# Performance work log

Hardware: AMD Instinct MI355X
Metric: run time of the kernel (lower is better)

The kernel has to match this reference:

```python
import jax, jax.numpy as jnp
import numpy as np

D_MODEL = 1024
NUM_HEADS = 16
HEAD_DIM = D_MODEL // NUM_HEADS
B, L = 2, 2048


def apply_rope(x, pos_emb):
    # x: [B,H,L,Dh], pos_emb: [1,1,L,Dh]
    x_even = x[..., ::2]
    x_odd = x[..., 1::2]
    cos = pos_emb[..., ::2]
    sin = pos_emb[..., 1::2]
    return jnp.concatenate([x_even * cos - x_odd * sin,
                            x_even * sin + x_odd * cos], axis=-1)


def setup_inputs() -> dict:
    key = jax.random.key(0)
    ks = jax.random.split(key, 13)
    s = D_MODEL ** -0.5
    return {
        'query': jax.random.normal(ks[0], (B, L, D_MODEL), jnp.float32),
        'key': jax.random.normal(ks[1], (B, L, D_MODEL), jnp.float32),
        'value': jax.random.normal(ks[2], (B, L, D_MODEL), jnp.float32),
        'alibi_bias': jax.random.normal(ks[3], (NUM_HEADS, L, L), jnp.float32),
        'pos_emb': jax.random.normal(ks[4], (1, 1, L, HEAD_DIM), jnp.float32),
        'Wq': jax.random.normal(ks[5], (D_MODEL, D_MODEL), jnp.float32) * s,
        'bq': jnp.zeros((D_MODEL,), jnp.float32),
        'Wk': jax.random.normal(ks[6], (D_MODEL, D_MODEL), jnp.float32) * s,
        'bk': jnp.zeros((D_MODEL,), jnp.float32),
        'Wv': jax.random.normal(ks[7], (D_MODEL, D_MODEL), jnp.float32) * s,
        'bv': jnp.zeros((D_MODEL,), jnp.float32),
        'Wo': jax.random.normal(ks[8], (D_MODEL, D_MODEL), jnp.float32) * s,
        'bo': jnp.zeros((D_MODEL,), jnp.float32),
    }


def reference(query, key, value, alibi_bias, pos_emb,
              Wq, bq, Wk, bk, Wv, bv, Wo, bo):
    scaling = HEAD_DIM ** -0.5
    Bq, Lq, _ = query.shape

    def proj(x, W, b):
        # torch Linear: x @ W.T + b -> [B,H,L,Dh]
        y = x @ W.T + b
        return y.reshape(Bq, Lq, NUM_HEADS, HEAD_DIM).transpose(0, 2, 1, 3)

    q = proj(query, Wq, bq)
    k = proj(key, Wk, bk)
    v = proj(value, Wv, bv)

    q = apply_rope(q, pos_emb)
    k = apply_rope(k, pos_emb)

    scores = jnp.einsum('bhqd,bhkd->bhqk', q, k) * scaling
    scores = scores + alibi_bias[None]
    attn = jax.nn.softmax(scores, axis=-1)
    out = jnp.einsum('bhqk,bhkd->bhqd', attn, v)
    out = out.transpose(0, 2, 1, 3).reshape(Bq, Lq, D_MODEL)
    return out @ Wo.T + bo
```

## Files before the change

### kernel.cpp

```cpp
#include <hip/hip_runtime.h>
#include <hip/hip_bf16.h>

#define DM 1024
#define NH 16
#define HD 64
#define BB 2
#define LLEN 2048
#define MR (BB*LLEN)

typedef __attribute__((ext_vector_type(8))) short bf16x8;
typedef __attribute__((ext_vector_type(4))) float f32x4;

#define AS1(p) ((const __attribute__((address_space(1))) void*)(p))
#define AS3(p) ((__attribute__((address_space(3))) void*)(p))

__device__ __forceinline__ ushort f2bf(float x) {
    union { float f; unsigned u; } v; v.f = x;
    unsigned r = v.u + 0x7FFFu + ((v.u >> 16) & 1u);
    return (ushort)(r >> 16);
}
__device__ __forceinline__ float bf2f(ushort x) {
    union { unsigned u; float f; } v; v.u = ((unsigned)x) << 16;
    return v.f;
}

__global__ __launch_bounds__(256) void cvtX(const float* __restrict__ a,
                                            const float* __restrict__ b,
                                            const float* __restrict__ c,
                                            ushort* __restrict__ dst, int n) {
    const float* src = blockIdx.y == 0 ? a : (blockIdx.y == 1 ? b : c);
    ushort* d = dst + (size_t)blockIdx.y * n;
    int i = (blockIdx.x * 256 + threadIdx.x) * 4;
    float4 v = *(const float4*)(src + i);
    ushort4 o = make_ushort4(f2bf(v.x), f2bf(v.y), f2bf(v.z), f2bf(v.w));
    *(ushort4*)(d + i) = o;
}

__global__ __launch_bounds__(256) void cvtW(const float* __restrict__ w0,
                                            const float* __restrict__ w1,
                                            const float* __restrict__ w2,
                                            const float* __restrict__ w3,
                                            ushort* __restrict__ dst, int n) {
    const float* src = blockIdx.y == 0 ? w0 : (blockIdx.y == 1 ? w1 : (blockIdx.y == 2 ? w2 : w3));
    ushort* d = dst + (size_t)blockIdx.y * n;
    int i = (blockIdx.x * 256 + threadIdx.x) * 4;
    float4 v = *(const float4*)(src + i);
    ushort4 o = make_ushort4(f2bf(v.x), f2bf(v.y), f2bf(v.z), f2bf(v.w));
    *(ushort4*)(d + i) = o;
}

template<typename OutT>
__global__ __launch_bounds__(256) void gemm_bt(
    const ushort* __restrict__ A, const ushort* __restrict__ Bw,
    OutT* __restrict__ Cc,
    const float* __restrict__ bias0, const float* __restrict__ bias1, const float* __restrict__ bias2,
    int M, int N, int K, long sA, long sB, long sC)
{
    __shared__ __attribute__((aligned(16))) ushort As[128 * 32];
    __shared__ __attribute__((aligned(16))) ushort Bs[128 * 32];
    const int tid = threadIdx.x;
    const int lane = tid & 63;
    const int wv = tid >> 6;
    const int wm = wv >> 1, wn = wv & 1;
    const int z = blockIdx.z;
    const ushort* Ab = A + (size_t)z * sA;
    const ushort* Bb = Bw + (size_t)z * sB;
    OutT* Cb = Cc + (size_t)z * sC;
    const float* bias = z == 0 ? bias0 : (z == 1 ? bias1 : bias2);
    const int m0 = blockIdx.x * 128;
    const int n0 = blockIdx.y * 128;
    const int l15 = lane & 15, l4 = lane >> 4;

    f32x4 acc[4][4] = {};
    const int nk = K >> 5;
    const int srow = tid >> 2;
    const int sblk = tid & 3;

    auto stage = [&](int kb) {
        int k0 = kb * 32;
#pragma unroll
        for (int r = 0; r < 2; ++r) {
            int row = r * 64 + srow;
            int s = (row >> 1) & 3;
            const ushort* ga = Ab + (size_t)(m0 + row) * K + k0 + ((sblk ^ s) * 8);
            __builtin_amdgcn_global_load_lds(AS1(ga), AS3(As + row * 32 + sblk * 8), 16, 0, 0);
            const ushort* gb = Bb + (size_t)(n0 + row) * K + k0 + ((sblk ^ s) * 8);
            __builtin_amdgcn_global_load_lds(AS1(gb), AS3(Bs + row * 32 + sblk * 8), 16, 0, 0);
        }
    };

    stage(0);
    for (int kb = 0; kb < nk; ++kb) {
        __syncthreads();
        bf16x8 af[4], bfr[4];
#pragma unroll
        for (int i = 0; i < 4; ++i) {
            int rowA = wm * 64 + i * 16 + l15;
            int sa = (rowA >> 1) & 3;
            af[i] = *(const bf16x8*)(As + rowA * 32 + ((l4 ^ sa) * 8));
            int rowB = wn * 64 + i * 16 + l15;
            int sb = (rowB >> 1) & 3;
            bfr[i] = *(const bf16x8*)(Bs + rowB * 32 + ((l4 ^ sb) * 8));
        }
#pragma unroll
        for (int i = 0; i < 4; ++i)
#pragma unroll
            for (int j = 0; j < 4; ++j)
                acc[i][j] = __builtin_amdgcn_mfma_f32_16x16x32_bf16(af[i], bfr[j], acc[i][j], 0, 0, 0);
        __syncthreads();
        if (kb + 1 < nk) stage(kb + 1);
    }
#pragma unroll
    for (int i = 0; i < 4; ++i) {
#pragma unroll
        for (int j = 0; j < 4; ++j) {
            int col = n0 + wn * 64 + j * 16 + l15;
            float bv = bias[col];
#pragma unroll
            for (int r = 0; r < 4; ++r) {
                int row = m0 + wm * 64 + i * 16 + l4 * 4 + r;
                float val = acc[i][j][r] + bv;
                if constexpr (sizeof(OutT) == 2) {
                    ((ushort*)Cb)[(size_t)row * N + col] = f2bf(val);
                } else {
                    Cb[(size_t)row * N + col] = val;
                }
            }
        }
    }
}

__global__ __launch_bounds__(256) void rope_qk(const ushort* __restrict__ Yq,
                                               const ushort* __restrict__ Yk,
                                               const float* __restrict__ pe,
                                               ushort* __restrict__ Qr,
                                               ushort* __restrict__ Kr) {
    int idx = blockIdx.x * 256 + threadIdx.x;
    int t = idx & 31;
    int h = (idx >> 5) & 15;
    int lq = (idx >> 9) & 2047;
    int b = idx >> 20;
    size_t srcoff = ((size_t)(b * LLEN + lq)) * DM + h * 64 + 2 * t;
    float2 cs = *(const float2*)(pe + (size_t)lq * 64 + 2 * t);
    unsigned yq = *(const unsigned*)(Yq + srcoff);
    unsigned yk = *(const unsigned*)(Yk + srcoff);
    float qe = bf2f((ushort)(yq & 0xffff)), qo = bf2f((ushort)(yq >> 16));
    float ke = bf2f((ushort)(yk & 0xffff)), ko = bf2f((ushort)(yk >> 16));
    size_t dst = ((size_t)(b * NH + h) * LLEN + lq) * 64;
    Qr[dst + t]      = f2bf(qe * cs.x - qo * cs.y);
    Qr[dst + 32 + t] = f2bf(qe * cs.y + qo * cs.x);
    Kr[dst + t]      = f2bf(ke * cs.x - ko * cs.y);
    Kr[dst + 32 + t] = f2bf(ke * cs.y + ko * cs.x);
}

__global__ __launch_bounds__(256) void vtrans(const ushort* __restrict__ Yv, ushort* __restrict__ Vt) {
    __shared__ __attribute__((aligned(16))) ushort Vs[64 * 66];
    int tid = threadIdx.x;
    int lb = blockIdx.x * 64;
    int bh = blockIdx.y;
    int b = bh >> 4, h = bh & 15;
#pragma unroll
    for (int p = 0; p < 2; ++p) {
        int lr = p * 32 + (tid >> 3);
        int cb = tid & 7;
        bf16x8 v = *(const bf16x8*)(Yv + (size_t)(b * LLEN + lb + lr) * DM + h * 64 + cb * 8);
#pragma unroll
        for (int j = 0; j < 8; ++j)
            Vs[(cb * 8 + j) * 66 + lr] = (ushort)v[j];
    }
    __syncthreads();
    int d = tid >> 2, part = tid & 3;
    unsigned w[8];
#pragma unroll
    for (int i = 0; i < 8; ++i) {
        unsigned lo = Vs[d * 66 + part * 16 + 2 * i];
        unsigned hi = Vs[d * 66 + part * 16 + 2 * i + 1];
        w[i] = lo | (hi << 16);
    }
    size_t dst = ((size_t)(bh * 64 + d)) * LLEN + lb + part * 16;
    uint4 o0 = make_uint4(w[0], w[1], w[2], w[3]);
    uint4 o1 = make_uint4(w[4], w[5], w[6], w[7]);
    *(uint4*)(Vt + dst) = o0;
    *(uint4*)(Vt + dst + 8) = o1;
}

__global__ __launch_bounds__(256) void attn(
    const ushort* __restrict__ Qr, const ushort* __restrict__ Kr, const ushort* __restrict__ Vt,
    const float* __restrict__ alibi, ushort* __restrict__ Abuf)
{
    __shared__ __attribute__((aligned(16))) ushort Ps[4][16 * 72];
    const float SCALE = 0.125f;
    int tid = threadIdx.x, lane = tid & 63, w = tid >> 6;
    int l15 = lane & 15, l4 = lane >> 4;
    int b = w >> 1, wq = w & 1;
    int h = blockIdx.y;
    int qb = blockIdx.x * 32 + wq * 16;
    int bh = b * NH + h;

    const ushort* Qb = Qr + ((size_t)bh * LLEN) * 64;
    const ushort* Kb = Kr + ((size_t)bh * LLEN) * 64;
    const ushort* Vb = Vt + ((size_t)bh * 64) * LLEN;
    const float* ab = alibi + (size_t)h * LLEN * LLEN;

    bf16x8 qf0 = *(const bf16x8*)(Qb + (size_t)(qb + l15) * 64 + l4 * 8);
    bf16x8 qf1 = *(const bf16x8*)(Qb + (size_t)(qb + l15) * 64 + 32 + l4 * 8);

    f32x4 O[4] = {};
    float mreg[4] = {-1e30f, -1e30f, -1e30f, -1e30f};
    float lreg[4] = {0.f, 0.f, 0.f, 0.f};
    ushort* Pw = &Ps[w][0];

    for (int kb = 0; kb < LLEN; kb += 64) {
        f32x4 s[4];
#pragma unroll
        for (int t = 0; t < 4; ++t) {
            const ushort* kr = Kb + (size_t)(kb + t * 16 + l15) * 64;
            bf16x8 kf0 = *(const bf16x8*)(kr + l4 * 8);
            bf16x8 kf1 = *(const bf16x8*)(kr + 32 + l4 * 8);
            f32x4 zz = {};
            zz = __builtin_amdgcn_mfma_f32_16x16x32_bf16(qf0, kf0, zz, 0, 0, 0);
            s[t] = __builtin_amdgcn_mfma_f32_16x16x32_bf16(qf1, kf1, zz, 0, 0, 0);
        }
        float sv[4][4];
#pragma unroll
        for (int t = 0; t < 4; ++t) {
            const float* ar = ab + (size_t)(qb + l4 * 4) * LLEN + kb + t * 16 + l15;
#pragma unroll
            for (int r = 0; r < 4; ++r)
                sv[t][r] = s[t][r] * SCALE + ar[(size_t)r * LLEN];
        }
        float mnew[4], fac[4];
#pragma unroll
        for (int r = 0; r < 4; ++r) {
            float mx = fmaxf(fmaxf(sv[0][r], sv[1][r]), fmaxf(sv[2][r], sv[3][r]));
            mx = fmaxf(mx, __shfl_xor(mx, 1));
            mx = fmaxf(mx, __shfl_xor(mx, 2));
            mx = fmaxf(mx, __shfl_xor(mx, 4));
            mx = fmaxf(mx, __shfl_xor(mx, 8));
            mnew[r] = fmaxf(mreg[r], mx);
            fac[r] = __expf(mreg[r] - mnew[r]);
            mreg[r] = mnew[r];
        }
#pragma unroll
        for (int r = 0; r < 4; ++r) {
            float rs = 0.f;
#pragma unroll
            for (int t = 0; t < 4; ++t) {
                float p = __expf(sv[t][r] - mreg[r]);
                sv[t][r] = p;
                rs += p;
            }
            rs += __shfl_xor(rs, 1);
            rs += __shfl_xor(rs, 2);
            rs += __shfl_xor(rs, 4);
            rs += __shfl_xor(rs, 8);
            lreg[r] = lreg[r] * fac[r] + rs;
        }
#pragma unroll
        for (int t = 0; t < 4; ++t)
#pragma unroll
            for (int r = 0; r < 4; ++r)
                Pw[(l4 * 4 + r) * 72 + t * 16 + l15] = f2bf(sv[t][r]);
#pragma unroll
        for (int dt = 0; dt < 4; ++dt)
#pragma unroll
            for (int r = 0; r < 4; ++r)
                O[dt][r] *= fac[r];
        bf16x8 pf0 = *(const bf16x8*)(Pw + l15 * 72 + l4 * 8);
        bf16x8 pf1 = *(const bf16x8*)(Pw + l15 * 72 + 32 + l4 * 8);
#pragma unroll
        for (int dt = 0; dt < 4; ++dt) {
            const ushort* vr = Vb + (size_t)(dt * 16 + l15) * LLEN + kb;
            bf16x8 vf0 = *(const bf16x8*)(vr + l4 * 8);
            bf16x8 vf1 = *(const bf16x8*)(vr + 32 + l4 * 8);
            O[dt] = __builtin_amdgcn_mfma_f32_16x16x32_bf16(pf0, vf0, O[dt], 0, 0, 0);
            O[dt] = __builtin_amdgcn_mfma_f32_16x16x32_bf16(pf1, vf1, O[dt], 0, 0, 0);
        }
    }
#pragma unroll
    for (int dt = 0; dt < 4; ++dt)
#pragma unroll
        for (int r = 0; r < 4; ++r) {
            int q = qb + l4 * 4 + r;
            float val = O[dt][r] / lreg[r];
            Abuf[(size_t)(b * LLEN + q) * DM + h * 64 + dt * 16 + l15] = f2bf(val);
        }
}

extern "C" void kernel_launch(void* const* d_in, const int* in_sizes, int n_in,
                              void* d_out, int out_size, void* d_ws, size_t ws_size,
                              hipStream_t stream) {
    const float* query = (const float*)d_in[0];
    const float* key_  = (const float*)d_in[1];
    const float* value = (const float*)d_in[2];
    const float* alibi = (const float*)d_in[3];
    const float* pose  = (const float*)d_in[4];
    const float* Wq    = (const float*)d_in[5];
    const float* bq    = (const float*)d_in[6];
    const float* Wk    = (const float*)d_in[7];
    const float* bk    = (const float*)d_in[8];
    const float* Wv    = (const float*)d_in[9];
    const float* bv    = (const float*)d_in[10];
    const float* Wo    = (const float*)d_in[11];
    const float* bo    = (const float*)d_in[12];

    ushort* Xbf  = (ushort*)d_ws;
    ushort* Wbf  = Xbf + 3UL * MR * DM;
    ushort* Ybf  = Wbf + 4UL * DM * DM;
    ushort* Qr   = Ybf + 3UL * MR * DM;
    ushort* Kr   = Qr + (size_t)BB * NH * LLEN * HD;
    ushort* Vt   = Kr + (size_t)BB * NH * LLEN * HD;
    ushort* Abuf = Vt + (size_t)BB * NH * LLEN * HD;

    cvtX<<<dim3(4096, 3), 256, 0, stream>>>(query, key_, value, Xbf, MR * DM);
    cvtW<<<dim3(1024, 4), 256, 0, stream>>>(Wq, Wk, Wv, Wo, Wbf, DM * DM);

    gemm_bt<ushort><<<dim3(32, 8, 3), 256, 0, stream>>>(
        Xbf, Wbf, Ybf, bq, bk, bv, MR, DM, DM,
        (long)MR * DM, (long)DM * DM, (long)MR * DM);

    rope_qk<<<8192, 256, 0, stream>>>(Ybf, Ybf + (size_t)MR * DM, pose, Qr, Kr);
    vtrans<<<dim3(32, 32), 256, 0, stream>>>(Ybf + 2UL * MR * DM, Vt);

    attn<<<dim3(LLEN / 32, NH), 256, 0, stream>>>(Qr, Kr, Vt, alibi, Abuf);

    gemm_bt<float><<<dim3(32, 8, 1), 256, 0, stream>>>(
        Abuf, Wbf + 3UL * DM * DM, (float*)d_out, bo, bo, bo, MR, DM, DM, 0, 0, 0);
}
```

Baseline: 701.3 us.

## Split attention over the key dimension and merge partial softmax results

Attention now runs as two key-range halves in separate blocks, each writing unnormalized fp32 partial outputs plus running max and sum. A new combine kernel rescales the two halves and writes the normalized bf16 output. The grid of 1024 blocks becomes 2048 to fill more compute units. The softmax scale and log2(e) are folded into Q during RoPE so the inner loop can use exp2 with a single fma for the alibi term. Costs are extra fp32 traffic for the partials (which reuse workspace buffers), one more launch, and a launch-bounds hint that may limit registers.

```diff
diff --git a/kernel.cpp b/kernel.cpp
--- a/kernel.cpp
+++ b/kernel.cpp
@@ -135,6 +135,7 @@
                                                const float* __restrict__ pe,
                                                ushort* __restrict__ Qr,
                                                ushort* __restrict__ Kr) {
+    const float QS = 0.125f * 1.44269504f;
     int idx = blockIdx.x * 256 + threadIdx.x;
     int t = idx & 31;
     int h = (idx >> 5) & 15;
@@ -147,8 +148,8 @@
     float qe = bf2f((ushort)(yq & 0xffff)), qo = bf2f((ushort)(yq >> 16));
     float ke = bf2f((ushort)(yk & 0xffff)), ko = bf2f((ushort)(yk >> 16));
     size_t dst = ((size_t)(b * NH + h) * LLEN + lq) * 64;
-    Qr[dst + t]      = f2bf(qe * cs.x - qo * cs.y);
-    Qr[dst + 32 + t] = f2bf(qe * cs.y + qo * cs.x);
+    Qr[dst + t]      = f2bf((qe * cs.x - qo * cs.y) * QS);
+    Qr[dst + 32 + t] = f2bf((qe * cs.y + qo * cs.x) * QS);
     Kr[dst + t]      = f2bf(ke * cs.x - ko * cs.y);
     Kr[dst + 32 + t] = f2bf(ke * cs.y + ko * cs.x);
 }
@@ -184,18 +185,21 @@
     *(uint4*)(Vt + dst + 8) = o1;
 }
 
-__global__ __launch_bounds__(256) void attn(
+__global__ __launch_bounds__(256, 8) void attn(
     const ushort* __restrict__ Qr, const ushort* __restrict__ Kr, const ushort* __restrict__ Vt,
-    const float* __restrict__ alibi, ushort* __restrict__ Abuf)
+    const float* __restrict__ alibi, float* __restrict__ O1, float* __restrict__ O2,
+    float2* __restrict__ Ml)
 {
     __shared__ __attribute__((aligned(16))) ushort Ps[4][16 * 72];
-    const float SCALE = 0.125f;
+    const float LOG2E = 1.44269504f;
     int tid = threadIdx.x, lane = tid & 63, w = tid >> 6;
     int l15 = lane & 15, l4 = lane >> 4;
     int b = w >> 1, wq = w & 1;
     int h = blockIdx.y;
+    int z = blockIdx.z;
     int qb = blockIdx.x * 32 + wq * 16;
     int bh = b * NH + h;
+    int kb0 = z * (LLEN / 2);
 
     const ushort* Qb = Qr + ((size_t)bh * LLEN) * 64;
     const ushort* Kb = Kr + ((size_t)bh * LLEN) * 64;
@@ -210,7 +214,7 @@
     float lreg[4] = {0.f, 0.f, 0.f, 0.f};
     ushort* Pw = &Ps[w][0];
 
-    for (int kb = 0; kb < LLEN; kb += 64) {
+    for (int kb = kb0; kb < kb0 + LLEN / 2; kb += 64) {
         f32x4 s[4];
 #pragma unroll
         for (int t = 0; t < 4; ++t) {
@@ -227,9 +231,9 @@
             const float* ar = ab + (size_t)(qb + l4 * 4) * LLEN + kb + t * 16 + l15;
 #pragma unroll
             for (int r = 0; r < 4; ++r)
-                sv[t][r] = s[t][r] * SCALE + ar[(size_t)r * LLEN];
-        }
-        float mnew[4], fac[4];
+                sv[t][r] = fmaf(ar[(size_t)r * LLEN], LOG2E, s[t][r]);
+        }
+        float fac[4];
 #pragma unroll
         for (int r = 0; r < 4; ++r) {
             float mx = fmaxf(fmaxf(sv[0][r], sv[1][r]), fmaxf(sv[2][r], sv[3][r]));
@@ -237,16 +241,16 @@
             mx = fmaxf(mx, __shfl_xor(mx, 2));
             mx = fmaxf(mx, __shfl_xor(mx, 4));
             mx = fmaxf(mx, __shfl_xor(mx, 8));
-            mnew[r] = fmaxf(mreg[r], mx);
-            fac[r] = __expf(mreg[r] - mnew[r]);
-            mreg[r] = mnew[r];
+            float mnew = fmaxf(mreg[r], mx);
+            fac[r] = exp2f(mreg[r] - mnew);
+            mreg[r] = mnew;
         }
 #pragma unroll
         for (int r = 0; r < 4; ++r) {
             float rs = 0.f;
 #pragma unroll
             for (int t = 0; t < 4; ++t) {
-                float p = __expf(sv[t][r] - mreg[r]);
+                float p = exp2f(sv[t][r] - mreg[r]);
                 sv[t][r] = p;
                 rs += p;
             }
@@ -277,14 +281,47 @@
             O[dt] = __builtin_amdgcn_mfma_f32_16x16x32_bf16(pf1, vf1, O[dt], 0, 0, 0);
         }
     }
+    float* Op = (z == 0) ? O1 : O2;
 #pragma unroll
     for (int dt = 0; dt < 4; ++dt)
 #pragma unroll
         for (int r = 0; r < 4; ++r) {
             int q = qb + l4 * 4 + r;
-            float val = O[dt][r] / lreg[r];
-            Abuf[(size_t)(b * LLEN + q) * DM + h * 64 + dt * 16 + l15] = f2bf(val);
-        }
+            Op[((size_t)bh * LLEN + q) * 64 + dt * 16 + l15] = O[dt][r];
+        }
+    if (l15 == 0) {
+#pragma unroll
+        for (int r = 0; r < 4; ++r) {
+            int q = qb + l4 * 4 + r;
+            Ml[((size_t)z * BB * NH + bh) * LLEN + q] = make_float2(mreg[r], lreg[r]);
+        }
+    }
+}
+
+__global__ __launch_bounds__(256) void combine(
+    const float* __restrict__ O1, const float* __restrict__ O2,
+    const float2* __restrict__ Ml, ushort* __restrict__ Abuf)
+{
+    int idx = blockIdx.x * 256 + threadIdx.x;
+    int d4 = idx & 15;
+    int q  = (idx >> 4) & (LLEN - 1);
+    int bh = idx >> 15;
+    int b = bh >> 4, h = bh & 15;
+    float2 ml1 = Ml[(size_t)bh * LLEN + q];
+    float2 ml2 = Ml[(size_t)(BB * NH + bh) * LLEN + q];
+    float m = fmaxf(ml1.x, ml2.x);
+    float w1 = exp2f(ml1.x - m);
+    float w2 = exp2f(ml2.x - m);
+    float inv = 1.0f / (ml1.y * w1 + ml2.y * w2);
+    size_t off = ((size_t)bh * LLEN + q) * 64 + d4 * 4;
+    float4 a = *(const float4*)(O1 + off);
+    float4 c = *(const float4*)(O2 + off);
+    ushort4 o;
+    o.x = f2bf((a.x * w1 + c.x * w2) * inv);
+    o.y = f2bf((a.y * w1 + c.y * w2) * inv);
+    o.z = f2bf((a.z * w1 + c.z * w2) * inv);
+    o.w = f2bf((a.w * w1 + c.w * w2) * inv);
+    *(ushort4*)(Abuf + ((size_t)(b * LLEN + q)) * DM + h * 64 + d4 * 4) = o;
 }
 
 extern "C" void kernel_launch(void* const* d_in, const int* in_sizes, int n_in,
@@ -312,6 +349,10 @@
     ushort* Vt   = Kr + (size_t)BB * NH * LLEN * HD;
     ushort* Abuf = Vt + (size_t)BB * NH * LLEN * HD;
 
+    float*  O1 = (float*)Xbf;
+    float2* Ml = (float2*)(Xbf + 9UL * 1024 * 1024);
+    float*  O2 = (float*)Ybf;
+
     cvtX<<<dim3(4096, 3), 256, 0, stream>>>(query, key_, value, Xbf, MR * DM);
     cvtW<<<dim3(1024, 4), 256, 0, stream>>>(Wq, Wk, Wv, Wo, Wbf, DM * DM);
 
@@ -322,7 +363,8 @@
     rope_qk<<<8192, 256, 0, stream>>>(Ybf, Ybf + (size_t)MR * DM, pose, Qr, Kr);
     vtrans<<<dim3(32, 32), 256, 0, stream>>>(Ybf + 2UL * MR * DM, Vt);
 
-    attn<<<dim3(LLEN / 32, NH), 256, 0, stream>>>(Qr, Kr, Vt, alibi, Abuf);
+    attn<<<dim3(LLEN / 32, NH, 2), 256, 0, stream>>>(Qr, Kr, Vt, alibi, O1, O2, Ml);
+    combine<<<4096, 256, 0, stream>>>(O1, O2, Ml, Abuf);
 
     gemm_bt<float><<<dim3(32, 8, 1), 256, 0, stream>>>(
         Abuf, Wbf + 3UL * DM * DM, (float*)d_out, bo, bo, bo, MR, DM, DM, 0, 0, 0);
```

New measurement: 839.7 us. 19.7% more time.
